# Kernel tuning notes

Measured on AMD Instinct MI355X. Metric: run time of the kernel, lower is better.

Reference implementation:

```python
import jax, jax.numpy as jnp
import numpy as np

N, C, G = 50000, 30, 1000   # cells, classes, genes
E = 800000                   # edges
OUT = 8                      # GATv2 out channels, heads=1


def setup_inputs() -> dict:
    key = jax.random.key(0)
    ks = jax.random.split(key, 12)
    X = jax.random.normal(ks[0], (N, G), dtype=jnp.float32)
    Mu = jax.random.normal(ks[1], (C, G), dtype=jnp.float32)
    Var = jax.random.uniform(ks[2], (C, G), dtype=jnp.float32) + 0.5  # strictly positive
    edge_index = jax.random.randint(ks[3], (2, E), 0, N, dtype=jnp.int64)
    # learned params
    W = 0.01 * jax.random.normal(ks[4], (N, C), dtype=jnp.float32)   # torch init zeros; small noise for nontrivial P
    S = jnp.ones((N, 1), dtype=jnp.float32)
    sc = 1.0 / np.sqrt(G)
    Wl = sc * jax.random.normal(ks[5], (OUT, G), dtype=jnp.float32)  # lin_l weight
    bl = jnp.zeros((OUT,), dtype=jnp.float32)
    Wr = sc * jax.random.normal(ks[6], (OUT, G), dtype=jnp.float32)  # lin_r weight
    br = jnp.zeros((OUT,), dtype=jnp.float32)
    att = jax.random.normal(ks[7], (OUT,), dtype=jnp.float32) / np.sqrt(OUT)
    return {"X": X, "Mu": Mu, "Var": Var, "edge_index": edge_index,
            "W": W, "S": S, "Wl": Wl, "bl": bl, "Wr": Wr, "br": br, "att": att}


def reference(X, Mu, Var, edge_index, W, S, Wl, bl, Wr, br, att):
    n = X.shape[0]
    P = jax.nn.softmax(W, axis=1)                       # [N,C]
    # Gaussian log-likelihood term. Expand (X - Mu*S)^2/Var summed over genes:
    invVar = 1.0 / Var                                  # [C,G]
    A = (X * X) @ invVar.T                              # [N,C]  sum X^2/Var
    B = X @ (Mu * invVar).T                             # [N,C]  sum X*Mu/Var
    D = jnp.sum(Mu * Mu * invVar, axis=1)               # [C]    sum Mu^2/Var
    Fmat = -0.5 * (A - 2.0 * S * B + (S * S) * D[None, :])  # [N,C]
    ll_prot = jnp.sum(P * Fmat) / n

    # GATv2 attention (heads=1, add_self_loops=False)
    x_l = X @ Wl.T + bl                                 # [N,8] source transform
    x_r = X @ Wr.T + br                                 # [N,8] target transform
    src, dst = edge_index[0], edge_index[1]
    m = jax.nn.leaky_relu(x_l[src] + x_r[dst], negative_slope=0.2)  # [E,8]
    e = m @ att                                         # [E]
    # edge-softmax grouped by destination node
    emax = jax.ops.segment_max(e, dst, num_segments=n)  # [N]
    e_exp = jnp.exp(e - emax[dst])                      # [E]
    denom = jax.ops.segment_sum(e_exp, dst, num_segments=n)  # [N]
    alpha = e_exp / (denom[dst] + 1e-16)                # [E]

    ce_space = -jnp.sum(P[src] * alpha[:, None] * jnp.log(P[dst] + 1e-8)) / n
    return ll_prot, ce_space, P
```

## Files before the change

### kernel.cpp

```cpp
#include <hip/hip_runtime.h>
#include <math.h>

#define N_CELLS 50000
#define C_CLS   30
#define G_GENES 1000
#define E_EDGES 800000
#define KPAD    1024
#define NREP    4

typedef __attribute__((ext_vector_type(8))) short bf16x8;
typedef __attribute__((ext_vector_type(4))) float f32x4;

__device__ __forceinline__ unsigned f2bf_u(float f) {
    unsigned u = __float_as_uint(f);
    return (u + 0x7fffu + ((u >> 16) & 1u)) >> 16;
}
__device__ __forceinline__ unsigned pack2(float lo, float hi) {
    return f2bf_u(lo) | (f2bf_u(hi) << 16);
}
__device__ __forceinline__ float bf2f(unsigned short u) {
    return __uint_as_float(((unsigned)u) << 16);
}

__device__ __forceinline__ float lrelu02(float v) { return v > 0.f ? v : 0.2f * v; }

__device__ __forceinline__ float dp4(int4 a, int4 b) {
    const unsigned* ua = (const unsigned*)&a;
    const unsigned* ub = (const unsigned*)&b;
    float s = 0.f;
#pragma unroll
    for (int i = 0; i < 4; i++) {
        float al = __uint_as_float(ua[i] << 16);
        float ah = __uint_as_float(ua[i] & 0xffff0000u);
        float bl = __uint_as_float(ub[i] << 16);
        float bh = __uint_as_float(ub[i] & 0xffff0000u);
        s += al * bl + ah * bh;
    }
    return s;
}

__global__ void prep_kernel(const float* __restrict__ Mu, const float* __restrict__ Var,
                            const float* __restrict__ Wl, const float* __restrict__ Wr,
                            unsigned short* __restrict__ CoefB, float* __restrict__ Dvec,
                            float* __restrict__ denom4, float* __restrict__ out) {
    const int r = blockIdx.x;
    const int t = threadIdx.x;
    __shared__ float red[256];
    float dacc = 0.f;
    for (int g = t; g < KPAD; g += 256) {
        float v = 0.f;
        if (g < G_GENES) {
            if (r < 30) {
                float iv = 1.0f / Var[r * G_GENES + g];
                float mu = Mu[r * G_GENES + g];
                v = iv;
                dacc += mu * mu * iv;
            } else if (r >= 32) {
                int i = r - 32;
                if (i < 30)      v = Mu[i * G_GENES + g] / Var[i * G_GENES + g];
                else if (i < 38) v = Wl[(i - 30) * G_GENES + g];
                else if (i < 46) v = Wr[(i - 38) * G_GENES + g];
            }
        }
        CoefB[r * KPAD + g] = (unsigned short)f2bf_u(v);
    }
    for (int i = blockIdx.x * 256 + t; i < N_CELLS * NREP; i += 80 * 256) denom4[i] = 0.f;
    if (r == 31 && t < 2) out[t] = 0.f;

    if (r < 30) {
        red[t] = dacc;
        __syncthreads();
        for (int s = 128; s > 0; s >>= 1) {
            if (t < s) red[t] += red[t + s];
            __syncthreads();
        }
        if (t == 0) Dvec[r] = red[0];
    }
}

__global__ __launch_bounds__(256, 4) void main_rows_kernel(
    const float* __restrict__ X, const float* __restrict__ W,
    const float* __restrict__ S, const float* __restrict__ bl,
    const float* __restrict__ br, const unsigned short* __restrict__ CoefB,
    const float* __restrict__ Dvec,
    float* __restrict__ out,
    unsigned short* __restrict__ Pb, unsigned short* __restrict__ Lb,
    float* __restrict__ xl, float* __restrict__ xr)
{
    __shared__ __align__(16) unsigned short Ct[80 * 72];

    const int t    = threadIdx.x;
    const int w    = t >> 6;
    const int l    = t & 63;
    const int l15  = l & 15;
    const int quad = l >> 4;
    const int k0q  = quad * 8;
    const int wavebase = blockIdx.x * 64 + w * 16;
    const bool valid = (wavebase < N_CELLS);
    const float* __restrict__ xrow = X + (size_t)(wavebase + l15) * G_GENES;

    f32x4 acc[5];
#pragma unroll
    for (int i = 0; i < 5; i++) acc[i] = (f32x4){0.f, 0.f, 0.f, 0.f};

    float4 c0a = make_float4(0,0,0,0), c0b = c0a, c1a = c0a, c1b = c0a;
    if (valid) {
        c0a = *(const float4*)&xrow[k0q];
        c0b = *(const float4*)&xrow[k0q + 4];
        c1a = *(const float4*)&xrow[32 + k0q];
        c1b = *(const float4*)&xrow[32 + k0q + 4];
    }

    for (int kt = 0; kt < KPAD; kt += 64) {
        __syncthreads();
        for (int u = t; u < 640; u += 256) {
            int row = u >> 3;
            int kk  = (u & 7) * 8;
            *(int4*)&Ct[row * 72 + kk] = *(const int4*)&CoefB[row * KPAD + kt + kk];
        }
        __syncthreads();

        float4 n0a = make_float4(0,0,0,0), n0b = n0a, n1a = n0a, n1b = n0a;
        const int ktn = kt + 64;
        if (valid && ktn < KPAD) {
            const int ka = ktn + k0q;
            n0a = *(const float4*)&xrow[ka];
            n0b = *(const float4*)&xrow[ka + 4];
            const int kb = ktn + 32 + k0q;
            if (kb < G_GENES) {
                n1a = *(const float4*)&xrow[kb];
                n1b = *(const float4*)&xrow[kb + 4];
            }
        }

        union { unsigned u[4]; bf16x8 v; } ua, u2;
        ua.u[0] = pack2(c0a.x, c0a.y); ua.u[1] = pack2(c0a.z, c0a.w);
        ua.u[2] = pack2(c0b.x, c0b.y); ua.u[3] = pack2(c0b.z, c0b.w);
        u2.u[0] = pack2(c0a.x * c0a.x, c0a.y * c0a.y);
        u2.u[1] = pack2(c0a.z * c0a.z, c0a.w * c0a.w);
        u2.u[2] = pack2(c0b.x * c0b.x, c0b.y * c0b.y);
        u2.u[3] = pack2(c0b.z * c0b.z, c0b.w * c0b.w);
#pragma unroll
        for (int nt = 0; nt < 5; nt++) {
            bf16x8 b = *(const bf16x8*)&Ct[(nt * 16 + l15) * 72 + k0q];
            acc[nt] = __builtin_amdgcn_mfma_f32_16x16x32_bf16(
                nt < 2 ? u2.v : ua.v, b, acc[nt], 0, 0, 0);
        }
        ua.u[0] = pack2(c1a.x, c1a.y); ua.u[1] = pack2(c1a.z, c1a.w);
        ua.u[2] = pack2(c1b.x, c1b.y); ua.u[3] = pack2(c1b.z, c1b.w);
        u2.u[0] = pack2(c1a.x * c1a.x, c1a.y * c1a.y);
        u2.u[1] = pack2(c1a.z * c1a.z, c1a.w * c1a.w);
        u2.u[2] = pack2(c1b.x * c1b.x, c1b.y * c1b.y);
        u2.u[3] = pack2(c1b.z * c1b.z, c1b.w * c1b.w);
#pragma unroll
        for (int nt = 0; nt < 5; nt++) {
            bf16x8 b = *(const bf16x8*)&Ct[(nt * 16 + l15) * 72 + 32 + k0q];
            acc[nt] = __builtin_amdgcn_mfma_f32_16x16x32_bf16(
                nt < 2 ? u2.v : ua.v, b, acc[nt], 0, 0, 0);
        }

        c0a = n0a; c0b = n0b; c1a = n1a; c1b = n1b;
    }

    if (!valid) return;

    const int rbase = wavebase + quad * 4;
    const bool c2ok = (l15 < 14);
    const float d0 = Dvec[l15];
    const float d1 = c2ok ? Dvec[16 + l15] : 0.f;
    float llacc = 0.f;
#pragma unroll
    for (int r = 0; r < 4; r++) {
        const int row = rbase + r;
        float w0 = W[(size_t)row * 30 + l15];
        float w1 = c2ok ? W[(size_t)row * 30 + 16 + l15] : -1e30f;
        float m = fmaxf(w0, w1);
#pragma unroll
        for (int mm = 1; mm < 16; mm <<= 1) m = fmaxf(m, __shfl_xor(m, mm, 64));
        float e0 = __expf(w0 - m);
        float e1 = c2ok ? __expf(w1 - m) : 0.f;
        float s = e0 + e1;
#pragma unroll
        for (int mm = 1; mm < 16; mm <<= 1) s += __shfl_xor(s, mm, 64);
        float inv = 1.0f / s;
        float p0 = e0 * inv, p1 = e1 * inv;
        float Sn = S[row], Sn2 = Sn * Sn;
        float F0 = -0.5f * (acc[0][r] - 2.0f * Sn * acc[2][r] + Sn2 * d0);
        float F1 = -0.5f * (acc[1][r] - 2.0f * Sn * acc[3][r] + Sn2 * d1);
        float lp = p0 * F0 + (c2ok ? p1 * F1 : 0.f);
#pragma unroll
        for (int mm = 1; mm < 16; mm <<= 1) lp += __shfl_xor(lp, mm, 64);
        llacc += lp;

        out[2 + (size_t)row * 30 + l15] = p0;
        float lg0 = __logf(p0 + 1e-8f);
        Pb[(size_t)row * 32 + l15] = (unsigned short)f2bf_u(p0);
        Lb[(size_t)row * 32 + l15] = (unsigned short)f2bf_u(lg0);
        if (c2ok) {
            out[2 + (size_t)row * 30 + 16 + l15] = p1;
            float lg1 = __logf(p1 + 1e-8f);
            Pb[(size_t)row * 32 + 16 + l15] = (unsigned short)f2bf_u(p1);
            Lb[(size_t)row * 32 + 16 + l15] = (unsigned short)f2bf_u(lg1);
        } else {
            Pb[(size_t)row * 32 + 16 + l15] = 0;
            Lb[(size_t)row * 32 + 16 + l15] = 0;
        }
        if (l15 >= 14)                xl[(size_t)row * 8 + (l15 - 14)] = acc[3][r] + bl[l15 - 14];
        else if (l15 < 6)             xl[(size_t)row * 8 + (l15 + 2)]  = acc[4][r] + bl[l15 + 2];
        if (l15 >= 6 && l15 < 14)     xr[(size_t)row * 8 + (l15 - 6)]  = acc[4][r] + br[l15 - 6];
    }
    llacc += __shfl_xor(llacc, 16, 64);
    llacc += __shfl_xor(llacc, 32, 64);
    if (l == 0) atomicAdd(&out[0], llacc * (1.0f / N_CELLS));
}

__global__ void edge_passA(const int* __restrict__ ei, const float* __restrict__ xl,
                           const float* __restrict__ xr, const float* __restrict__ att,
                           unsigned short* __restrict__ evalsB, float* __restrict__ denom4) {
    int e = blockIdx.x * 256 + threadIdx.x;
    if (e >= E_EDGES) return;
    int src = ei[e];
    int dst = ei[E_EDGES + e];
    const float4* lp = (const float4*)&xl[(size_t)src * 8];
    const float4* rp = (const float4*)&xr[(size_t)dst * 8];
    float4 l0 = lp[0], l1 = lp[1];
    float4 r0 = rp[0], r1 = rp[1];
    float ev = 0.f;
    ev += lrelu02(l0.x + r0.x) * att[0];
    ev += lrelu02(l0.y + r0.y) * att[1];
    ev += lrelu02(l0.z + r0.z) * att[2];
    ev += lrelu02(l0.w + r0.w) * att[3];
    ev += lrelu02(l1.x + r1.x) * att[4];
    ev += lrelu02(l1.y + r1.y) * att[5];
    ev += lrelu02(l1.z + r1.z) * att[6];
    ev += lrelu02(l1.w + r1.w) * att[7];
    float p = __expf(ev);
    evalsB[e] = (unsigned short)f2bf_u(p);
    atomicAdd(&denom4[(blockIdx.x & (NREP - 1)) * N_CELLS + dst], bf2f(f2bf_u(p)));
}

__global__ void reduce_denom(const float* __restrict__ denom4, float* __restrict__ denom) {
    int i = blockIdx.x * 256 + threadIdx.x;
    if (i < N_CELLS)
        denom[i] = (denom4[i] + denom4[N_CELLS + i]) +
                   (denom4[2 * N_CELLS + i] + denom4[3 * N_CELLS + i]);
}

__global__ __launch_bounds__(256) void edge_passB(
    const int* __restrict__ ei, const unsigned short* __restrict__ evalsB,
    const float* __restrict__ denom, const unsigned short* __restrict__ Pb,
    const unsigned short* __restrict__ Lb, float* __restrict__ out) {
    const int t = threadIdx.x;
    const int e = blockIdx.x * 256 + t;
    int src = ei[e];
    int dst = ei[E_EDGES + e];
    float alpha = bf2f(evalsB[e]) / (denom[dst] + 1e-16f);
    const int4* ps = (const int4*)&Pb[(size_t)src * 32];
    const int4* ld = (const int4*)&Lb[(size_t)dst * 32];
    int4 a0 = ps[0], a1 = ps[1], a2 = ps[2], a3 = ps[3];
    int4 b0 = ld[0], b1 = ld[1], b2 = ld[2], b3 = ld[3];
    float dot = dp4(a0, b0) + dp4(a1, b1) + dp4(a2, b2) + dp4(a3, b3);
    float contrib = -alpha * dot;

    for (int m = 1; m < 64; m <<= 1) contrib += __shfl_xor(contrib, m, 64);
    __shared__ float wsum[4];
    if ((t & 63) == 0) wsum[t >> 6] = contrib;
    __syncthreads();
    if (t == 0)
        atomicAdd(&out[1], (wsum[0] + wsum[1] + wsum[2] + wsum[3]) * (1.0f / N_CELLS));
}

extern "C" void kernel_launch(void* const* d_in, const int* in_sizes, int n_in,
                              void* d_out, int out_size, void* d_ws, size_t ws_size,
                              hipStream_t stream) {
    const float* X   = (const float*)d_in[0];
    const float* Mu  = (const float*)d_in[1];
    const float* Var = (const float*)d_in[2];
    const int*   ei  = (const int*)d_in[3];
    const float* W   = (const float*)d_in[4];
    const float* S   = (const float*)d_in[5];
    const float* Wl  = (const float*)d_in[6];
    const float* bl  = (const float*)d_in[7];
    const float* Wr  = (const float*)d_in[8];
    const float* br  = (const float*)d_in[9];
    const float* att = (const float*)d_in[10];

    float* out = (float*)d_out;

    float* wsf = (float*)d_ws;
    unsigned short* CoefB  = (unsigned short*)wsf;
    float* Dvec            = wsf + 40960;
    unsigned short* Pb     = (unsigned short*)(wsf + 40992);
    unsigned short* Lb     = (unsigned short*)(wsf + 840992);
    float* xl              = wsf + 1640992;
    float* xr              = wsf + 2040992;
    unsigned short* evalsB = (unsigned short*)(wsf + 2440992);
    float* denom           = wsf + 2840992;
    float* denom4          = wsf + 2890992;

    prep_kernel<<<80, 256, 0, stream>>>(Mu, Var, Wl, Wr, CoefB, Dvec, denom4, out);
    main_rows_kernel<<<(N_CELLS + 63) / 64, 256, 0, stream>>>(
        X, W, S, bl, br, CoefB, Dvec, out, Pb, Lb, xl, xr);
    edge_passA<<<(E_EDGES + 255) / 256, 256, 0, stream>>>(ei, xl, xr, att, evalsB, denom4);
    reduce_denom<<<(N_CELLS + 255) / 256, 256, 0, stream>>>(denom4, denom);
    edge_passB<<<E_EDGES / 256, 256, 0, stream>>>(ei, evalsB, denom, Pb, Lb, out);
}
```

Measured before the change: 450.2 us.

## Fuse edge passes via per-destination numerator/denominator accumulation and drop LDS staging

Rewrites the cross-entropy term as a per-destination sum: each edge atomically adds exp(e) and exp(e)*dot(P_src, logP_dst) into paired accumulators, and a finalize kernel divides numerator by denominator per node. This merges two edge passes and the denominator reduction into one edge pass plus one finalize pass, removing the stored edge values and the second read of the edge index. The main row kernel also drops its shared-memory staging of the coefficient matrix and its barriers, loading B fragments straight from global/L2, and lowers the occupancy hint. Doubling the atomics per edge adds contention, and exp without max subtraction was already present.

Measured after the change: 472.7 us. +5.0%, slower.

```diff
diff --git a/kernel.cpp b/kernel.cpp
--- a/kernel.cpp
+++ b/kernel.cpp
@@ -42,7 +42,7 @@
 __global__ void prep_kernel(const float* __restrict__ Mu, const float* __restrict__ Var,
                             const float* __restrict__ Wl, const float* __restrict__ Wr,
                             unsigned short* __restrict__ CoefB, float* __restrict__ Dvec,
-                            float* __restrict__ denom4, float* __restrict__ out) {
+                            float* __restrict__ dn4, float* __restrict__ out) {
     const int r = blockIdx.x;
     const int t = threadIdx.x;
     __shared__ float red[256];
@@ -64,7 +64,7 @@
         }
         CoefB[r * KPAD + g] = (unsigned short)f2bf_u(v);
     }
-    for (int i = blockIdx.x * 256 + t; i < N_CELLS * NREP; i += 80 * 256) denom4[i] = 0.f;
+    for (int i = blockIdx.x * 256 + t; i < N_CELLS * NREP * 2; i += 80 * 256) dn4[i] = 0.f;
     if (r == 31 && t < 2) out[t] = 0.f;
 
     if (r < 30) {
@@ -78,7 +78,7 @@
     }
 }
 
-__global__ __launch_bounds__(256, 4) void main_rows_kernel(
+__global__ __launch_bounds__(256, 3) void main_rows_kernel(
     const float* __restrict__ X, const float* __restrict__ W,
     const float* __restrict__ S, const float* __restrict__ bl,
     const float* __restrict__ br, const unsigned short* __restrict__ CoefB,
@@ -87,8 +87,6 @@
     unsigned short* __restrict__ Pb, unsigned short* __restrict__ Lb,
     float* __restrict__ xl, float* __restrict__ xr)
 {
-    __shared__ __align__(16) unsigned short Ct[80 * 72];
-
     const int t    = threadIdx.x;
     const int w    = t >> 6;
     const int l    = t & 63;
@@ -96,33 +94,24 @@
     const int quad = l >> 4;
     const int k0q  = quad * 8;
     const int wavebase = blockIdx.x * 64 + w * 16;
-    const bool valid = (wavebase < N_CELLS);
+    if (wavebase >= N_CELLS) return;
     const float* __restrict__ xrow = X + (size_t)(wavebase + l15) * G_GENES;
+    const unsigned short* __restrict__ cb = CoefB + (size_t)l15 * KPAD + k0q;
 
     f32x4 acc[5];
 #pragma unroll
     for (int i = 0; i < 5; i++) acc[i] = (f32x4){0.f, 0.f, 0.f, 0.f};
 
-    float4 c0a = make_float4(0,0,0,0), c0b = c0a, c1a = c0a, c1b = c0a;
-    if (valid) {
-        c0a = *(const float4*)&xrow[k0q];
-        c0b = *(const float4*)&xrow[k0q + 4];
-        c1a = *(const float4*)&xrow[32 + k0q];
-        c1b = *(const float4*)&xrow[32 + k0q + 4];
-    }
-
+    float4 c0a = *(const float4*)&xrow[k0q];
+    float4 c0b = *(const float4*)&xrow[k0q + 4];
+    float4 c1a = *(const float4*)&xrow[32 + k0q];
+    float4 c1b = *(const float4*)&xrow[32 + k0q + 4];
+
+#pragma unroll 2
     for (int kt = 0; kt < KPAD; kt += 64) {
-        __syncthreads();
-        for (int u = t; u < 640; u += 256) {
-            int row = u >> 3;
-            int kk  = (u & 7) * 8;
-            *(int4*)&Ct[row * 72 + kk] = *(const int4*)&CoefB[row * KPAD + kt + kk];
-        }
-        __syncthreads();
-
-        float4 n0a = make_float4(0,0,0,0), n0b = n0a, n1a = n0a, n1b = n0a;
+        float4 n0a = make_float4(0.f, 0.f, 0.f, 0.f), n0b = n0a, n1a = n0a, n1b = n0a;
         const int ktn = kt + 64;
-        if (valid && ktn < KPAD) {
+        if (ktn < KPAD) {
             const int ka = ktn + k0q;
             n0a = *(const float4*)&xrow[ka];
             n0b = *(const float4*)&xrow[ka + 4];
@@ -142,7 +131,7 @@
         u2.u[3] = pack2(c0b.z * c0b.z, c0b.w * c0b.w);
 #pragma unroll
         for (int nt = 0; nt < 5; nt++) {
-            bf16x8 b = *(const bf16x8*)&Ct[(nt * 16 + l15) * 72 + k0q];
+            bf16x8 b = *(const bf16x8*)&cb[(size_t)nt * 16 * KPAD + kt];
             acc[nt] = __builtin_amdgcn_mfma_f32_16x16x32_bf16(
                 nt < 2 ? u2.v : ua.v, b, acc[nt], 0, 0, 0);
         }
@@ -154,15 +143,13 @@
         u2.u[3] = pack2(c1b.z * c1b.z, c1b.w * c1b.w);
 #pragma unroll
         for (int nt = 0; nt < 5; nt++) {
-            bf16x8 b = *(const bf16x8*)&Ct[(nt * 16 + l15) * 72 + 32 + k0q];
+            bf16x8 b = *(const bf16x8*)&cb[(size_t)nt * 16 * KPAD + kt + 32];
             acc[nt] = __builtin_amdgcn_mfma_f32_16x16x32_bf16(
                 nt < 2 ? u2.v : ua.v, b, acc[nt], 0, 0, 0);
         }
 
         c0a = n0a; c0b = n0b; c1a = n1a; c1b = n1b;
     }
-
-    if (!valid) return;
 
     const int rbase = wavebase + quad * 4;
     const bool c2ok = (l15 < 14);
@@ -214,9 +201,11 @@
     if (l == 0) atomicAdd(&out[0], llacc * (1.0f / N_CELLS));
 }
 
-__global__ void edge_passA(const int* __restrict__ ei, const float* __restrict__ xl,
-                           const float* __restrict__ xr, const float* __restrict__ att,
-                           unsigned short* __restrict__ evalsB, float* __restrict__ denom4) {
+__global__ __launch_bounds__(256) void edge_pass(
+    const int* __restrict__ ei, const float* __restrict__ xl,
+    const float* __restrict__ xr, const float* __restrict__ att,
+    const unsigned short* __restrict__ Pb, const unsigned short* __restrict__ Lb,
+    float* __restrict__ dn4) {
     int e = blockIdx.x * 256 + threadIdx.x;
     if (e >= E_EDGES) return;
     int src = ei[e];
@@ -235,39 +224,37 @@
     ev += lrelu02(l1.z + r1.z) * att[6];
     ev += lrelu02(l1.w + r1.w) * att[7];
     float p = __expf(ev);
-    evalsB[e] = (unsigned short)f2bf_u(p);
-    atomicAdd(&denom4[(blockIdx.x & (NREP - 1)) * N_CELLS + dst], bf2f(f2bf_u(p)));
-}
-
-__global__ void reduce_denom(const float* __restrict__ denom4, float* __restrict__ denom) {
-    int i = blockIdx.x * 256 + threadIdx.x;
-    if (i < N_CELLS)
-        denom[i] = (denom4[i] + denom4[N_CELLS + i]) +
-                   (denom4[2 * N_CELLS + i] + denom4[3 * N_CELLS + i]);
-}
-
-__global__ __launch_bounds__(256) void edge_passB(
-    const int* __restrict__ ei, const unsigned short* __restrict__ evalsB,
-    const float* __restrict__ denom, const unsigned short* __restrict__ Pb,
-    const unsigned short* __restrict__ Lb, float* __restrict__ out) {
-    const int t = threadIdx.x;
-    const int e = blockIdx.x * 256 + t;
-    int src = ei[e];
-    int dst = ei[E_EDGES + e];
-    float alpha = bf2f(evalsB[e]) / (denom[dst] + 1e-16f);
+
     const int4* ps = (const int4*)&Pb[(size_t)src * 32];
     const int4* ld = (const int4*)&Lb[(size_t)dst * 32];
     int4 a0 = ps[0], a1 = ps[1], a2 = ps[2], a3 = ps[3];
     int4 b0 = ld[0], b1 = ld[1], b2 = ld[2], b3 = ld[3];
     float dot = dp4(a0, b0) + dp4(a1, b1) + dp4(a2, b2) + dp4(a3, b3);
-    float contrib = -alpha * dot;
-
-    for (int m = 1; m < 64; m <<= 1) contrib += __shfl_xor(contrib, m, 64);
+
+    float* base = &dn4[((size_t)(blockIdx.x & (NREP - 1)) * N_CELLS + dst) * 2];
+    atomicAdd(base, p);
+    atomicAdd(base + 1, p * dot);
+}
+
+__global__ __launch_bounds__(256) void finalize_kernel(const float* __restrict__ dn4,
+                                                       float* __restrict__ out) {
+    const int t = threadIdx.x;
+    const int i = blockIdx.x * 256 + t;
+    float c = 0.f;
+    if (i < N_CELLS) {
+        float d  = (dn4[(size_t)i * 2]     + dn4[((size_t)N_CELLS + i) * 2]) +
+                   (dn4[((size_t)2 * N_CELLS + i) * 2] + dn4[((size_t)3 * N_CELLS + i) * 2]);
+        float nm = (dn4[(size_t)i * 2 + 1] + dn4[((size_t)N_CELLS + i) * 2 + 1]) +
+                   (dn4[((size_t)2 * N_CELLS + i) * 2 + 1] + dn4[((size_t)3 * N_CELLS + i) * 2 + 1]);
+        c = nm / (d + 1e-16f);
+    }
+#pragma unroll
+    for (int m = 1; m < 64; m <<= 1) c += __shfl_xor(c, m, 64);
     __shared__ float wsum[4];
-    if ((t & 63) == 0) wsum[t >> 6] = contrib;
+    if ((t & 63) == 0) wsum[t >> 6] = c;
     __syncthreads();
     if (t == 0)
-        atomicAdd(&out[1], (wsum[0] + wsum[1] + wsum[2] + wsum[3]) * (1.0f / N_CELLS));
+        atomicAdd(&out[1], -(wsum[0] + wsum[1] + wsum[2] + wsum[3]) * (1.0f / N_CELLS));
 }
 
 extern "C" void kernel_launch(void* const* d_in, const int* in_sizes, int n_in,
@@ -294,14 +281,11 @@
     unsigned short* Lb     = (unsigned short*)(wsf + 840992);
     float* xl              = wsf + 1640992;
     float* xr              = wsf + 2040992;
-    unsigned short* evalsB = (unsigned short*)(wsf + 2440992);
-    float* denom           = wsf + 2840992;
-    float* denom4          = wsf + 2890992;
-
-    prep_kernel<<<80, 256, 0, stream>>>(Mu, Var, Wl, Wr, CoefB, Dvec, denom4, out);
+    float* dn4             = wsf + 2440992;
+
+    prep_kernel<<<80, 256, 0, stream>>>(Mu, Var, Wl, Wr, CoefB, Dvec, dn4, out);
     main_rows_kernel<<<(N_CELLS + 63) / 64, 256, 0, stream>>>(
         X, W, S, bl, br, CoefB, Dvec, out, Pb, Lb, xl, xr);
-    edge_passA<<<(E_EDGES + 255) / 256, 256, 0, stream>>>(ei, xl, xr, att, evalsB, denom4);
-    reduce_denom<<<(N_CELLS + 255) / 256, 256, 0, stream>>>(denom4, denom);
-    edge_passB<<<E_EDGES / 256, 256, 0, stream>>>(ei, evalsB, denom, Pb, Lb, out);
-}
+    edge_pass<<<(E_EDGES + 255) / 256, 256, 0, stream>>>(ei, xl, xr, att, Pb, Lb, dn4);
+    finalize_kernel<<<(N_CELLS + 255) / 256, 256, 0, stream>>>(dn4, out);
+}
```
